# Kernel optimization log

Hardware: AMD Instinct MI355X
Metric: run time of the kernel (lower is better)

The kernel has to match this reference:

```python
import jax, jax.numpy as jnp
import numpy as np

B, S, D = 2, 2048, 2048
H = 16
Q_LORA, KV_LORA = 1536, 512
ROPE_DIM, NOPE_DIM, V_DIM = 64, 64, 128
Q_HEAD_DIM = NOPE_DIM + ROPE_DIM  # 128
ROPE_THETA, ROPE_RATIO = 10000.0, 1.0


def setup_inputs() -> dict:
    key = jax.random.key(0)
    ks = jax.random.split(key, 6)
    std = 0.02
    return {
        "hidden_states": jax.random.normal(ks[0], (B, S, D), jnp.float32),
        "Wqa": jax.random.normal(ks[1], (D, Q_LORA), jnp.float32) * std,
        "Wqb": jax.random.normal(ks[2], (Q_LORA, H * Q_HEAD_DIM), jnp.float32) * std,
        "Wkva": jax.random.normal(ks[3], (D, KV_LORA + ROPE_DIM), jnp.float32) * std,
        "Wkvb": jax.random.normal(ks[4], (KV_LORA, H * (NOPE_DIM + V_DIM)), jnp.float32) * std,
        "Wo": jax.random.normal(ks[5], (H * V_DIM, D), jnp.float32) * std,
    }


def _rope_tables(seq_len):
    half = ROPE_DIM // 2
    inv_freq = ROPE_RATIO / (ROPE_THETA ** (jnp.arange(half, dtype=jnp.float32) * 2.0 / ROPE_DIM))
    freqs = jnp.arange(seq_len, dtype=jnp.float32)[:, None] * inv_freq[None, :]  # [S, half]
    return jnp.cos(freqs), jnp.sin(freqs)


def _apply_rope(x, cos, sin):
    # interleaved even/odd rotation, matches torch stack+flatten
    x_even = x[..., 0::2]
    x_odd = x[..., 1::2]
    r_even = x_even * cos - x_odd * sin
    r_odd = x_odd * cos + x_even * sin
    return jnp.stack([r_even, r_odd], axis=-1).reshape(x.shape)


def reference(hidden_states, Wqa, Wqb, Wkva, Wkvb, Wo):
    b, s, _ = hidden_states.shape
    scale = Q_HEAD_DIM ** -0.5

    # query compression path
    q_latent = hidden_states @ Wqa                             # [B,S,Q_LORA]
    q = (q_latent @ Wqb).reshape(b, s, H, Q_HEAD_DIM)
    q = jnp.transpose(q, (0, 2, 1, 3))                          # [B,H,S,q_head_dim]
    q_nope, q_pe = q[..., :NOPE_DIM], q[..., NOPE_DIM:]

    # kv compression
    kv_comp = hidden_states @ Wkva                              # [B,S,KV_LORA+ROPE]
    c_kv, k_pe = kv_comp[..., :KV_LORA], kv_comp[..., KV_LORA:]

    cos, sin = _rope_tables(s)                                  # [S, ROPE_DIM//2]
    q_pe = _apply_rope(q_pe, cos, sin)                          # [B,H,S,ROPE]
    k_pe = _apply_rope(k_pe, cos, sin)                          # [B,S,ROPE]

    # kv decompression
    kv = (c_kv @ Wkvb).reshape(b, s, H, NOPE_DIM + V_DIM)
    kv = jnp.transpose(kv, (0, 2, 1, 3))                        # [B,H,S,nope+v]
    k_nope, v = kv[..., :NOPE_DIM], kv[..., NOPE_DIM:]

    k_pe_b = jnp.broadcast_to(k_pe[:, None], (b, H, s, ROPE_DIM))
    q_full = jnp.concatenate([q_nope, q_pe], axis=-1)           # [B,H,S,128]
    k_full = jnp.concatenate([k_nope, k_pe_b], axis=-1)         # [B,H,S,128]

    scores = jnp.einsum('bhqd,bhkd->bhqk', q_full, k_full) * scale
    causal = jnp.tril(jnp.ones((s, s), dtype=bool))
    scores = jnp.where(causal[None, None], scores, jnp.finfo(scores.dtype).min)
    probs = jax.nn.softmax(scores, axis=-1)
    attn = jnp.einsum('bhqk,bhkd->bhqd', probs, v)              # [B,H,S,V_DIM]

    out = jnp.transpose(attn, (0, 2, 1, 3)).reshape(b, s, H * V_DIM)
    return out @ Wo                                             # [B,S,D]
```

## Files before the change

### kernel.cpp

```cpp
#include <hip/hip_runtime.h>
#include <hip/hip_bf16.h>
#include <cstdint>
#include <cstddef>

typedef __bf16 bf16_t;
typedef __attribute__((ext_vector_type(8))) __bf16 bf16x8;
typedef __attribute__((ext_vector_type(4))) float f32x4;

#define S_ 2048
#define H_ 16
#define NTOK 4096

__device__ __forceinline__ f32x4 mfma16x16(bf16x8 a, bf16x8 b, f32x4 c) {
  return __builtin_amdgcn_mfma_f32_16x16x32_bf16(a, b, c, 0, 0, 0);
}
__device__ __forceinline__ bf16x8 load8(const bf16_t* p) {
  return *reinterpret_cast<const bf16x8*>(p);
}
__device__ __forceinline__ void load_lds16(const void* g, void* l) {
  __builtin_amdgcn_global_load_lds(
      (const __attribute__((address_space(1))) uint32_t*)g,
      (__attribute__((address_space(3))) uint32_t*)l, 16, 0, 0);
}


__global__ void cast_bf16_k(const float* __restrict__ in, bf16_t* __restrict__ out, int n) {
  int idx = blockIdx.x * 256 + threadIdx.x;
  int i4 = idx * 4;
  if (i4 >= n) return;
  float4 v = *reinterpret_cast<const float4*>(in + i4);
  out[i4 + 0] = (bf16_t)v.x;
  out[i4 + 1] = (bf16_t)v.y;
  out[i4 + 2] = (bf16_t)v.z;
  out[i4 + 3] = (bf16_t)v.w;
}

__global__ void transpose_cast_k(const float* __restrict__ in, bf16_t* __restrict__ out,
                                 int K, int Nsrc, int Nout) {
  __shared__ float tile[32][33];
  int k0 = blockIdx.y * 32, n0 = blockIdx.x * 32;
  int tx = threadIdx.x & 31, ty = threadIdx.x >> 5;
#pragma unroll
  for (int i = 0; i < 4; ++i) {
    int k = k0 + ty + i * 8, n = n0 + tx;
    tile[ty + i * 8][tx] = (n < Nsrc) ? in[(size_t)k * Nsrc + n] : 0.0f;
  }
  __syncthreads();
#pragma unroll
  for (int i = 0; i < 4; ++i) {
    int n = n0 + ty + i * 8, k = k0 + tx;
    out[(size_t)n * K + k] = (bf16_t)tile[tx][ty + i * 8];
  }
}

__global__ void transpose_v_k(const bf16_t* __restrict__ kv, bf16_t* __restrict__ vT) {
  __shared__ bf16_t tile[32][33];
  int bh = blockIdx.z;
  int b = bh >> 4, h = bh & 15;
  int s0 = blockIdx.x * 32, d0 = blockIdx.y * 32;
  int tx = threadIdx.x & 31, ty = threadIdx.x >> 5;
#pragma unroll
  for (int i = 0; i < 4; ++i) {
    int s = s0 + ty + i * 8;
    tile[ty + i * 8][tx] = kv[(size_t)(b * S_ + s) * 3072 + h * 192 + 64 + d0 + tx];
  }
  __syncthreads();
#pragma unroll
  for (int i = 0; i < 4; ++i) {
    int d = d0 + ty + i * 8;
    vT[((size_t)bh * 128 + d) * 2048 + s0 + tx] = tile[tx][ty + i * 8];
  }
}

__global__ void rope_tables_k(float* __restrict__ cosT, float* __restrict__ sinT) {
  int idx = blockIdx.x * 256 + threadIdx.x;
  if (idx >= S_ * 32) return;
  int s = idx >> 5, i = idx & 31;
  float inv = powf(10000.0f, -(2.0f * (float)i) / 64.0f);
  float fr = (float)s * inv;
  cosT[idx] = cosf(fr);
  sinT[idx] = sinf(fr);
}

__global__ void rope_apply_k(bf16_t* __restrict__ buf, const float* __restrict__ cosT,
                             const float* __restrict__ sinT, int ld, int nh, int hstride, int off) {
  int idx = blockIdx.x * 256 + threadIdx.x;
  int total = NTOK * nh * 32;
  if (idx >= total) return;
  int i = idx & 31;
  int h = (idx >> 5) % nh;
  int t = idx / (32 * nh);
  int s = t & (S_ - 1);
  float c = cosT[s * 32 + i], sn = sinT[s * 32 + i];
  bf16_t* p = buf + (size_t)t * ld + off + h * hstride + 2 * i;
  float xe = (float)p[0], xo = (float)p[1];
  p[0] = (bf16_t)(xe * c - xo * sn);
  p[1] = (bf16_t)(xo * c + xe * sn);
}


template <int OUT_F32>
__global__ __launch_bounds__(256) void gemm_bf16(const bf16_t* __restrict__ A, int lda,
                                                 const bf16_t* __restrict__ Bt,
                                                 void* __restrict__ Cv, int M, int N, int K,
                                                 float scale) {
  __shared__ alignas(16) bf16_t Al[128 * 32];
  __shared__ alignas(16) bf16_t Bl[128 * 32];
  const int tid = threadIdx.x;
  const int wid = tid >> 6, lane = tid & 63;
  const int m0 = blockIdx.y * 128, n0 = blockIdx.x * 128;
  const int wm = (wid >> 1) * 64, wn = (wid & 1) * 64;

  f32x4 acc[4][4] = {};

  const int srow = wid * 32 + (lane >> 2);
  const int scol = (lane & 3) * 8;
  const bf16_t* ag0 = A + (size_t)(m0 + srow) * lda + scol;
  const bf16_t* ag1 = A + (size_t)(m0 + srow + 16) * lda + scol;
  const bf16_t* bg0 = Bt + (size_t)(n0 + srow) * K + scol;
  const bf16_t* bg1 = Bt + (size_t)(n0 + srow + 16) * K + scol;
  bf16_t* al0 = &Al[wid * 1024];
  bf16_t* al1 = &Al[wid * 1024 + 512];
  bf16_t* bl0 = &Bl[wid * 1024];
  bf16_t* bl1 = &Bl[wid * 1024 + 512];

  const int lr = lane & 15, lk = (lane >> 4) * 8;

  for (int k0 = 0; k0 < K; k0 += 32) {
    load_lds16(ag0 + k0, al0);
    load_lds16(ag1 + k0, al1);
    load_lds16(bg0 + k0, bl0);
    load_lds16(bg1 + k0, bl1);
    __syncthreads();
    bf16x8 af[4], bfr[4];
#pragma unroll
    for (int i = 0; i < 4; ++i) {
      af[i] = load8(&Al[(wm + i * 16 + lr) * 32 + lk]);
      bfr[i] = load8(&Bl[(wn + i * 16 + lr) * 32 + lk]);
    }
#pragma unroll
    for (int i = 0; i < 4; ++i)
#pragma unroll
      for (int j = 0; j < 4; ++j) acc[i][j] = mfma16x16(af[i], bfr[j], acc[i][j]);
    __syncthreads();
  }

  const int lg = lane >> 4;
  if (OUT_F32) {
    float* C = (float*)Cv;
#pragma unroll
    for (int i = 0; i < 4; ++i)
#pragma unroll
      for (int j = 0; j < 4; ++j)
#pragma unroll
        for (int r = 0; r < 4; ++r) {
          int row = m0 + wm + i * 16 + lg * 4 + r;
          int col = n0 + wn + j * 16 + lr;
          C[(size_t)row * N + col] = acc[i][j][r] * scale;
        }
  } else {
    bf16_t* C = (bf16_t*)Cv;
#pragma unroll
    for (int i = 0; i < 4; ++i)
#pragma unroll
      for (int j = 0; j < 4; ++j)
#pragma unroll
        for (int r = 0; r < 4; ++r) {
          int row = m0 + wm + i * 16 + lg * 4 + r;
          int col = n0 + wn + j * 16 + lr;
          C[(size_t)row * N + col] = (bf16_t)(acc[i][j][r] * scale);
        }
  }
}

__global__ __launch_bounds__(256) void attn_fused(const bf16_t* __restrict__ q,
                                                  const bf16_t* __restrict__ kv,
                                                  const bf16_t* __restrict__ lat,
                                                  const bf16_t* __restrict__ vT,
                                                  bf16_t* __restrict__ out) {
  __shared__ alignas(16) bf16_t Kn[64 * 64];
  __shared__ alignas(16) bf16_t Kp[64 * 64];
  __shared__ alignas(16) bf16_t Vt[128 * 64];
  __shared__ alignas(16) bf16_t Pl[4 * 16 * 64];
  const int tid = threadIdx.x, wid = tid >> 6, lane = tid & 63;
  const int bid = blockIdx.x;
  const int pairi = bid >> 5;
  const int bh = bid & 31;
  const int b = bh >> 4, h = bh & 15;
  const int tokb = b * S_;
  const int lr = lane & 15, lg = lane >> 4;
  const int srow8 = lane >> 3, c8 = lane & 7;
  const int swz8 = c8 ^ srow8;
  bf16_t* Pw = &Pl[wid * 1024];

  for (int phase = 0; phase < 2; ++phase) {
    const int qt = phase ? (31 - pairi) : pairi;

    bf16x8 qf[4];
    {
      const int qrow = qt * 64 + wid * 16 + lr;
      const bf16_t* qp = q + (size_t)(tokb + qrow) * 2048 + h * 128 + lg * 8;
#pragma unroll
      for (int ds = 0; ds < 4; ++ds) qf[ds] = load8(qp + ds * 32);
    }

    f32x4 o[8] = {};
    float mrow[4] = {-1e30f, -1e30f, -1e30f, -1e30f};
    float lrow[4] = {0.f, 0.f, 0.f, 0.f};

    for (int t = 0; t <= qt; ++t) {
      const int kb = t * 64;
#pragma unroll
      for (int rr = 0; rr < 2; ++rr) {
        const int r0 = wid * 16 + rr * 8;
        const int row = r0 + srow8;
        const size_t tk = (size_t)(tokb + kb + row);
        load_lds16(kv + tk * 3072 + h * 192 + (swz8 << 3), &Kn[r0 * 64]);
        load_lds16(lat + tk * 2176 + 2048 + (swz8 << 3), &Kp[r0 * 64]);
      }
#pragma unroll
      for (int rr = 0; rr < 4; ++rr) {
        const int r0 = wid * 32 + rr * 8;
        const int row = r0 + srow8;
        load_lds16(vT + ((size_t)bh * 128 + row) * 2048 + kb + (swz8 << 3), &Vt[r0 * 64]);
      }
      __syncthreads();

      f32x4 s[4];
#pragma unroll
      for (int kt = 0; kt < 4; ++kt) {
        const int row = kt * 16 + lr;
        const int e = lr & 7;
        bf16x8 kf0 = load8(&Kn[row * 64 + ((lg ^ e) << 3)]);
        bf16x8 kf1 = load8(&Kn[row * 64 + (((lg + 4) ^ e) << 3)]);
        bf16x8 kf2 = load8(&Kp[row * 64 + ((lg ^ e) << 3)]);
        bf16x8 kf3 = load8(&Kp[row * 64 + (((lg + 4) ^ e) << 3)]);
        f32x4 acc = {0.f, 0.f, 0.f, 0.f};
        acc = mfma16x16(qf[0], kf0, acc);
        acc = mfma16x16(qf[1], kf1, acc);
        acc = mfma16x16(qf[2], kf2, acc);
        acc = mfma16x16(qf[3], kf3, acc);
        s[kt] = acc;
      }

      if (t == qt) {
#pragma unroll
        for (int kt = 0; kt < 4; ++kt) {
          const int key = kb + kt * 16 + lr;
#pragma unroll
          for (int r = 0; r < 4; ++r) {
            const int qr = qt * 64 + wid * 16 + lg * 4 + r;
            if (key > qr) s[kt][r] = -1e30f;
          }
        }
      }

      float corr[4];
#pragma unroll
      for (int r = 0; r < 4; ++r) {
        float mx = fmaxf(fmaxf(s[0][r], s[1][r]), fmaxf(s[2][r], s[3][r]));
        mx = fmaxf(mx, __shfl_xor(mx, 1));
        mx = fmaxf(mx, __shfl_xor(mx, 2));
        mx = fmaxf(mx, __shfl_xor(mx, 4));
        mx = fmaxf(mx, __shfl_xor(mx, 8));
        float mn = fmaxf(mrow[r], mx);
        corr[r] = __expf(mrow[r] - mn);
        mrow[r] = mn;
      }
      float psum[4] = {0.f, 0.f, 0.f, 0.f};
#pragma unroll
      for (int kt = 0; kt < 4; ++kt)
#pragma unroll
        for (int r = 0; r < 4; ++r) {
          float p = __expf(s[kt][r] - mrow[r]);
          s[kt][r] = p;
          psum[r] += p;
        }
#pragma unroll
      for (int r = 0; r < 4; ++r) {
        float ps = psum[r];
        ps += __shfl_xor(ps, 1);
        ps += __shfl_xor(ps, 2);
        ps += __shfl_xor(ps, 4);
        ps += __shfl_xor(ps, 8);
        lrow[r] = lrow[r] * corr[r] + ps;
      }
#pragma unroll
      for (int n = 0; n < 8; ++n)
#pragma unroll
        for (int r = 0; r < 4; ++r) o[n][r] *= corr[r];

#pragma unroll
      for (int kt = 0; kt < 4; ++kt)
#pragma unroll
        for (int r = 0; r < 4; ++r) {
          const int qrow = lg * 4 + r;
          const int key = kt * 16 + lr;
          Pw[qrow * 64 + ((((key >> 3) ^ (qrow & 7)) << 3) | (key & 7))] = (bf16_t)s[kt][r];
        }

#pragma unroll
      for (int ks = 0; ks < 2; ++ks) {
        const int e = lr & 7;
        bf16x8 pa = load8(&Pw[lr * 64 + (((ks * 4 + lg) ^ e) << 3)]);
#pragma unroll
        for (int n = 0; n < 8; ++n) {
          bf16x8 vb = load8(&Vt[(n * 16 + lr) * 64 + (((ks * 4 + lg) ^ e) << 3)]);
          o[n] = mfma16x16(pa, vb, o[n]);
        }
      }
      __syncthreads();
    }

#pragma unroll
    for (int n = 0; n < 8; ++n)
#pragma unroll
      for (int r = 0; r < 4; ++r) {
        const int qr = qt * 64 + wid * 16 + lg * 4 + r;
        float val = o[n][r] / lrow[r];
        out[(size_t)(tokb + qr) * 2048 + h * 128 + n * 16 + lr] = (bf16_t)val;
      }
  }
}


extern "C" void kernel_launch(void* const* d_in, const int* in_sizes, int n_in, void* d_out,
                              int out_size, void* d_ws, size_t ws_size, hipStream_t stream) {
  const float* hs = (const float*)d_in[0];
  const float* Wqa = (const float*)d_in[1];
  const float* Wqb = (const float*)d_in[2];
  const float* Wkva = (const float*)d_in[3];
  const float* Wkvb = (const float*)d_in[4];
  const float* Wo = (const float*)d_in[5];
  float* out = (float*)d_out;

  char* ws = (char*)d_ws;
  size_t off = 0;
  auto alloc = [&](size_t bytes) {
    void* p = ws + off;
    off += (bytes + 255) & ~(size_t)255;
    return p;
  };
  bf16_t* hsb = (bf16_t*)alloc((size_t)NTOK * 2048 * 2);
  bf16_t* W1t = (bf16_t*)alloc((size_t)2176 * 2048 * 2);
  bf16_t* Wqbt = (bf16_t*)alloc((size_t)2048 * 1536 * 2);
  bf16_t* Wkvbt = (bf16_t*)alloc((size_t)3072 * 512 * 2);
  bf16_t* Wot = (bf16_t*)alloc((size_t)2048 * 2048 * 2);
  bf16_t* lat = (bf16_t*)alloc((size_t)NTOK * 2176 * 2);
  bf16_t* qb = (bf16_t*)alloc((size_t)NTOK * 2048 * 2);
  bf16_t* kvb = (bf16_t*)alloc((size_t)NTOK * 3072 * 2);
  bf16_t* attn = (bf16_t*)alloc((size_t)NTOK * 2048 * 2);
  bf16_t* vT = (bf16_t*)alloc((size_t)32 * 128 * 2048 * 2);
  float* cosT = (float*)alloc((size_t)S_ * 32 * 4);
  float* sinT = (float*)alloc((size_t)S_ * 32 * 4);

  cast_bf16_k<<<(NTOK * 2048 / 4 + 255) / 256, 256, 0, stream>>>(hs, hsb, NTOK * 2048);
  transpose_cast_k<<<dim3(1536 / 32, 2048 / 32), 256, 0, stream>>>(Wqa, W1t, 2048, 1536, 1536);
  transpose_cast_k<<<dim3(640 / 32, 2048 / 32), 256, 0, stream>>>(Wkva, W1t + (size_t)1536 * 2048,
                                                                  2048, 576, 640);
  transpose_cast_k<<<dim3(2048 / 32, 1536 / 32), 256, 0, stream>>>(Wqb, Wqbt, 1536, 2048, 2048);
  transpose_cast_k<<<dim3(3072 / 32, 512 / 32), 256, 0, stream>>>(Wkvb, Wkvbt, 512, 3072, 3072);
  transpose_cast_k<<<dim3(2048 / 32, 2048 / 32), 256, 0, stream>>>(Wo, Wot, 2048, 2048, 2048);
  rope_tables_k<<<(S_ * 32 + 255) / 256, 256, 0, stream>>>(cosT, sinT);

  gemm_bf16<0><<<dim3(2176 / 128, NTOK / 128), 256, 0, stream>>>(hsb, 2048, W1t, lat, NTOK, 2176,
                                                                 2048, 1.0f);
  rope_apply_k<<<(NTOK * 32 + 255) / 256, 256, 0, stream>>>(lat, cosT, sinT, 2176, 1, 0, 2048);
  const float scale = 0.08838834764831845f;
  gemm_bf16<0><<<dim3(2048 / 128, NTOK / 128), 256, 0, stream>>>(lat, 2176, Wqbt, qb, NTOK, 2048,
                                                                 1536, scale);
  rope_apply_k<<<(NTOK * 16 * 32 + 255) / 256, 256, 0, stream>>>(qb, cosT, sinT, 2048, 16, 128, 64);
  gemm_bf16<0><<<dim3(3072 / 128, NTOK / 128), 256, 0, stream>>>(lat + 1536, 2176, Wkvbt, kvb, NTOK,
                                                                 3072, 512, 1.0f);
  transpose_v_k<<<dim3(64, 4, 32), 256, 0, stream>>>(kvb, vT);
  attn_fused<<<dim3(512), 256, 0, stream>>>(qb, kvb, lat, vT, attn);
  gemm_bf16<1><<<dim3(2048 / 128, NTOK / 128), 256, 0, stream>>>(attn, 2048, Wot, out, NTOK, 2048,
                                                                 2048, 1.0f);
}
```

Measured before the change: 328.5 us.

## Split attention into one q-tile per block, lazy rescale, exp2 softmax

Replaces the paired q-tile loop with one q-tile per block (1024 blocks) and a zig-zag ordering of tiles so heavy causal tiles are scheduled first. Folds log2(e) into the Q scale so softmax uses exp2, skips the running-max rescale unless the max grows by more than a threshold, and raises wave priority around the MFMA sections. It aims to improve load balance and occupancy and to cut exponential and rescale ALU work. The lazy rescale relies on the accumulators staying in range when the max lags.

```diff
diff --git a/kernel.cpp b/kernel.cpp
--- a/kernel.cpp
+++ b/kernel.cpp
@@ -181,146 +181,155 @@
   __shared__ alignas(16) bf16_t Kn[64 * 64];
   __shared__ alignas(16) bf16_t Kp[64 * 64];
   __shared__ alignas(16) bf16_t Vt[128 * 64];
-  __shared__ alignas(16) bf16_t Pl[4 * 16 * 64];
+  __shared__ alignas(16) bf16_t Pl[4][16 * 64];
   const int tid = threadIdx.x, wid = tid >> 6, lane = tid & 63;
   const int bid = blockIdx.x;
-  const int pairi = bid >> 5;
+  const int g = bid >> 8;
+  const int x = (bid >> 5) & 7;
   const int bh = bid & 31;
+  const int qt = (g & 1) ? (24 - g * 8 + x) : (31 - g * 8 - x);
   const int b = bh >> 4, h = bh & 15;
   const int tokb = b * S_;
   const int lr = lane & 15, lg = lane >> 4;
   const int srow8 = lane >> 3, c8 = lane & 7;
   const int swz8 = c8 ^ srow8;
-  bf16_t* Pw = &Pl[wid * 1024];
-
-  for (int phase = 0; phase < 2; ++phase) {
-    const int qt = phase ? (31 - pairi) : pairi;
-
-    bf16x8 qf[4];
-    {
-      const int qrow = qt * 64 + wid * 16 + lr;
-      const bf16_t* qp = q + (size_t)(tokb + qrow) * 2048 + h * 128 + lg * 8;
-#pragma unroll
-      for (int ds = 0; ds < 4; ++ds) qf[ds] = load8(qp + ds * 32);
-    }
-
-    f32x4 o[8] = {};
-    float mrow[4] = {-1e30f, -1e30f, -1e30f, -1e30f};
-    float lrow[4] = {0.f, 0.f, 0.f, 0.f};
-
-    for (int t = 0; t <= qt; ++t) {
-      const int kb = t * 64;
-#pragma unroll
-      for (int rr = 0; rr < 2; ++rr) {
-        const int r0 = wid * 16 + rr * 8;
-        const int row = r0 + srow8;
-        const size_t tk = (size_t)(tokb + kb + row);
-        load_lds16(kv + tk * 3072 + h * 192 + (swz8 << 3), &Kn[r0 * 64]);
-        load_lds16(lat + tk * 2176 + 2048 + (swz8 << 3), &Kp[r0 * 64]);
-      }
-#pragma unroll
-      for (int rr = 0; rr < 4; ++rr) {
-        const int r0 = wid * 32 + rr * 8;
-        const int row = r0 + srow8;
-        load_lds16(vT + ((size_t)bh * 128 + row) * 2048 + kb + (swz8 << 3), &Vt[r0 * 64]);
-      }
-      __syncthreads();
-
-      f32x4 s[4];
+  bf16_t* Pw = &Pl[wid][0];
+
+  bf16x8 qf[4];
+  {
+    const int qrow = qt * 64 + wid * 16 + lr;
+    const bf16_t* qp = q + (size_t)(tokb + qrow) * 2048 + h * 128 + lg * 8;
+#pragma unroll
+    for (int ds = 0; ds < 4; ++ds) qf[ds] = load8(qp + ds * 32);
+  }
+
+  f32x4 o[8] = {};
+  float mrow[4] = {-1e30f, -1e30f, -1e30f, -1e30f};
+  float lrow[4] = {0.f, 0.f, 0.f, 0.f};
+
+  for (int t = 0; t <= qt; ++t) {
+    const int kb = t * 64;
+#pragma unroll
+    for (int rr = 0; rr < 2; ++rr) {
+      const int r0 = wid * 16 + rr * 8;
+      const size_t tk = (size_t)(tokb + kb + r0 + srow8);
+      load_lds16(kv + tk * 3072 + h * 192 + (swz8 << 3), &Kn[r0 * 64]);
+      load_lds16(lat + tk * 2176 + 2048 + (swz8 << 3), &Kp[r0 * 64]);
+    }
+#pragma unroll
+    for (int rr = 0; rr < 4; ++rr) {
+      const int r0 = wid * 32 + rr * 8;
+      load_lds16(vT + ((size_t)bh * 128 + r0 + srow8) * 2048 + kb + (swz8 << 3), &Vt[r0 * 64]);
+    }
+    __syncthreads();
+
+    f32x4 s[4];
+    __builtin_amdgcn_s_setprio(1);
+#pragma unroll
+    for (int kt = 0; kt < 4; ++kt) {
+      const int row = kt * 16 + lr;
+      const int e = lr & 7;
+      bf16x8 kf0 = load8(&Kn[row * 64 + ((lg ^ e) << 3)]);
+      bf16x8 kf1 = load8(&Kn[row * 64 + (((lg + 4) ^ e) << 3)]);
+      bf16x8 kf2 = load8(&Kp[row * 64 + ((lg ^ e) << 3)]);
+      bf16x8 kf3 = load8(&Kp[row * 64 + (((lg + 4) ^ e) << 3)]);
+      f32x4 acc = {0.f, 0.f, 0.f, 0.f};
+      acc = mfma16x16(qf[0], kf0, acc);
+      acc = mfma16x16(qf[1], kf1, acc);
+      acc = mfma16x16(qf[2], kf2, acc);
+      acc = mfma16x16(qf[3], kf3, acc);
+      s[kt] = acc;
+    }
+    __builtin_amdgcn_s_setprio(0);
+
+    if (t == qt) {
 #pragma unroll
       for (int kt = 0; kt < 4; ++kt) {
-        const int row = kt * 16 + lr;
-        const int e = lr & 7;
-        bf16x8 kf0 = load8(&Kn[row * 64 + ((lg ^ e) << 3)]);
-        bf16x8 kf1 = load8(&Kn[row * 64 + (((lg + 4) ^ e) << 3)]);
-        bf16x8 kf2 = load8(&Kp[row * 64 + ((lg ^ e) << 3)]);
-        bf16x8 kf3 = load8(&Kp[row * 64 + (((lg + 4) ^ e) << 3)]);
-        f32x4 acc = {0.f, 0.f, 0.f, 0.f};
-        acc = mfma16x16(qf[0], kf0, acc);
-        acc = mfma16x16(qf[1], kf1, acc);
-        acc = mfma16x16(qf[2], kf2, acc);
-        acc = mfma16x16(qf[3], kf3, acc);
-        s[kt] = acc;
-      }
-
-      if (t == qt) {
-#pragma unroll
-        for (int kt = 0; kt < 4; ++kt) {
-          const int key = kb + kt * 16 + lr;
-#pragma unroll
-          for (int r = 0; r < 4; ++r) {
-            const int qr = qt * 64 + wid * 16 + lg * 4 + r;
-            if (key > qr) s[kt][r] = -1e30f;
-          }
+        const int key = kb + kt * 16 + lr;
+#pragma unroll
+        for (int r = 0; r < 4; ++r) {
+          const int qr = qt * 64 + wid * 16 + lg * 4 + r;
+          if (key > qr) s[kt][r] = -1e30f;
         }
       }
-
-      float corr[4];
+    }
+
+    float tm[4];
+#pragma unroll
+    for (int r = 0; r < 4; ++r) {
+      float mx = fmaxf(fmaxf(s[0][r], s[1][r]), fmaxf(s[2][r], s[3][r]));
+      mx = fmaxf(mx, __shfl_xor(mx, 1));
+      mx = fmaxf(mx, __shfl_xor(mx, 2));
+      mx = fmaxf(mx, __shfl_xor(mx, 4));
+      mx = fmaxf(mx, __shfl_xor(mx, 8));
+      tm[r] = mx;
+    }
+    float need = fmaxf(fmaxf(tm[0] - mrow[0], tm[1] - mrow[1]),
+                       fmaxf(tm[2] - mrow[2], tm[3] - mrow[3]));
+    if (!__all(need <= 8.0f)) {
 #pragma unroll
       for (int r = 0; r < 4; ++r) {
-        float mx = fmaxf(fmaxf(s[0][r], s[1][r]), fmaxf(s[2][r], s[3][r]));
-        mx = fmaxf(mx, __shfl_xor(mx, 1));
-        mx = fmaxf(mx, __shfl_xor(mx, 2));
-        mx = fmaxf(mx, __shfl_xor(mx, 4));
-        mx = fmaxf(mx, __shfl_xor(mx, 8));
-        float mn = fmaxf(mrow[r], mx);
-        corr[r] = __expf(mrow[r] - mn);
+        float mn = fmaxf(mrow[r], tm[r]);
+        float corr = exp2f(mrow[r] - mn);
         mrow[r] = mn;
-      }
-      float psum[4] = {0.f, 0.f, 0.f, 0.f};
-#pragma unroll
-      for (int kt = 0; kt < 4; ++kt)
-#pragma unroll
-        for (int r = 0; r < 4; ++r) {
-          float p = __expf(s[kt][r] - mrow[r]);
-          s[kt][r] = p;
-          psum[r] += p;
-        }
+        lrow[r] *= corr;
+#pragma unroll
+        for (int n = 0; n < 8; ++n) o[n][r] *= corr;
+      }
+    }
+    float psum[4] = {0.f, 0.f, 0.f, 0.f};
+#pragma unroll
+    for (int kt = 0; kt < 4; ++kt)
 #pragma unroll
       for (int r = 0; r < 4; ++r) {
-        float ps = psum[r];
-        ps += __shfl_xor(ps, 1);
-        ps += __shfl_xor(ps, 2);
-        ps += __shfl_xor(ps, 4);
-        ps += __shfl_xor(ps, 8);
-        lrow[r] = lrow[r] * corr[r] + ps;
-      }
-#pragma unroll
-      for (int n = 0; n < 8; ++n)
-#pragma unroll
-        for (int r = 0; r < 4; ++r) o[n][r] *= corr[r];
-
-#pragma unroll
-      for (int kt = 0; kt < 4; ++kt)
-#pragma unroll
-        for (int r = 0; r < 4; ++r) {
-          const int qrow = lg * 4 + r;
-          const int key = kt * 16 + lr;
-          Pw[qrow * 64 + ((((key >> 3) ^ (qrow & 7)) << 3) | (key & 7))] = (bf16_t)s[kt][r];
-        }
-
-#pragma unroll
-      for (int ks = 0; ks < 2; ++ks) {
-        const int e = lr & 7;
-        bf16x8 pa = load8(&Pw[lr * 64 + (((ks * 4 + lg) ^ e) << 3)]);
-#pragma unroll
-        for (int n = 0; n < 8; ++n) {
-          bf16x8 vb = load8(&Vt[(n * 16 + lr) * 64 + (((ks * 4 + lg) ^ e) << 3)]);
-          o[n] = mfma16x16(pa, vb, o[n]);
-        }
-      }
-      __syncthreads();
-    }
-
-#pragma unroll
-    for (int n = 0; n < 8; ++n)
+        float p = exp2f(s[kt][r] - mrow[r]);
+        s[kt][r] = p;
+        psum[r] += p;
+      }
+#pragma unroll
+    for (int r = 0; r < 4; ++r) {
+      float ps = psum[r];
+      ps += __shfl_xor(ps, 1);
+      ps += __shfl_xor(ps, 2);
+      ps += __shfl_xor(ps, 4);
+      ps += __shfl_xor(ps, 8);
+      lrow[r] += ps;
+    }
+
+#pragma unroll
+    for (int kt = 0; kt < 4; ++kt)
 #pragma unroll
       for (int r = 0; r < 4; ++r) {
-        const int qr = qt * 64 + wid * 16 + lg * 4 + r;
-        float val = o[n][r] / lrow[r];
-        out[(size_t)(tokb + qr) * 2048 + h * 128 + n * 16 + lr] = (bf16_t)val;
-      }
-  }
+        const int qrow = lg * 4 + r;
+        const int key = kt * 16 + lr;
+        Pw[qrow * 64 + ((((key >> 3) ^ (qrow & 7)) << 3) | (key & 7))] = (bf16_t)s[kt][r];
+      }
+
+    __builtin_amdgcn_s_setprio(1);
+#pragma unroll
+    for (int ks = 0; ks < 2; ++ks) {
+      const int e = lr & 7;
+      bf16x8 pa = load8(&Pw[lr * 64 + (((ks * 4 + lg) ^ e) << 3)]);
+#pragma unroll
+      for (int n = 0; n < 8; ++n) {
+        bf16x8 vb = load8(&Vt[(n * 16 + lr) * 64 + (((ks * 4 + lg) ^ e) << 3)]);
+        o[n] = mfma16x16(pa, vb, o[n]);
+      }
+    }
+    __builtin_amdgcn_s_setprio(0);
+    __syncthreads();
+  }
+
+  float linv[4];
+#pragma unroll
+  for (int r = 0; r < 4; ++r) linv[r] = __builtin_amdgcn_rcpf(lrow[r]);
+#pragma unroll
+  for (int n = 0; n < 8; ++n)
+#pragma unroll
+    for (int r = 0; r < 4; ++r) {
+      const int qr = qt * 64 + wid * 16 + lg * 4 + r;
+      out[(size_t)(tokb + qr) * 2048 + h * 128 + n * 16 + lr] = (bf16_t)(o[n][r] * linv[r]);
+    }
 }
 
 
@@ -366,14 +375,14 @@
   gemm_bf16<0><<<dim3(2176 / 128, NTOK / 128), 256, 0, stream>>>(hsb, 2048, W1t, lat, NTOK, 2176,
                                                                  2048, 1.0f);
   rope_apply_k<<<(NTOK * 32 + 255) / 256, 256, 0, stream>>>(lat, cosT, sinT, 2176, 1, 0, 2048);
-  const float scale = 0.08838834764831845f;
+  const float scale = 0.08838834764831845f * 1.4426950408889634f;
   gemm_bf16<0><<<dim3(2048 / 128, NTOK / 128), 256, 0, stream>>>(lat, 2176, Wqbt, qb, NTOK, 2048,
                                                                  1536, scale);
   rope_apply_k<<<(NTOK * 16 * 32 + 255) / 256, 256, 0, stream>>>(qb, cosT, sinT, 2048, 16, 128, 64);
   gemm_bf16<0><<<dim3(3072 / 128, NTOK / 128), 256, 0, stream>>>(lat + 1536, 2176, Wkvbt, kvb, NTOK,
                                                                  3072, 512, 1.0f);
   transpose_v_k<<<dim3(64, 4, 32), 256, 0, stream>>>(kvb, vT);
-  attn_fused<<<dim3(512), 256, 0, stream>>>(qb, kvb, lat, vT, attn);
+  attn_fused<<<dim3(1024), 256, 0, stream>>>(qb, kvb, lat, vT, attn);
   gemm_bf16<1><<<dim3(2048 / 128, NTOK / 128), 256, 0, stream>>>(attn, 2048, Wot, out, NTOK, 2048,
                                                                  2048, 1.0f);
 }
```

After: 325.9 us. No clear change (-0.8%).
